# Optimization experiments

Hardware: AMD Instinct MI355X
Metric: run time of the kernel (lower is better)

## Reference

```python
import jax, jax.numpy as jnp
import numpy as np

TOP_K = 2  # cfg.MODEL.MOE.TOP_K


def setup_inputs() -> dict:
    key = jax.random.key(0)
    ks = jax.random.split(key, 5)
    bs, L, d_in, d_out, E = 32, 1024, 768, 256, 8
    return {
        "x": jax.random.normal(ks[0], (bs, L, d_in), dtype=jnp.float32),
        "gate_W": jax.random.normal(ks[1], (d_in, E), dtype=jnp.float32) * (1.0 / np.sqrt(d_in)),
        "gate_b": jax.random.normal(ks[2], (E,), dtype=jnp.float32) * 0.01,
        "expert_W": jax.random.normal(ks[3], (E, d_in, d_out), dtype=jnp.float32) * (1.0 / np.sqrt(d_in)),
        "expert_b": jax.random.normal(ks[4], (E, d_out), dtype=jnp.float32) * 0.01,
    }


def reference(x, gate_W, gate_b, expert_W, expert_b):
    # Gate: (bs, L, E) softmax over experts, then top-k routing weights.
    gate_logits = jnp.einsum("bli,ie->ble", x, gate_W) + gate_b
    gate_weights = jax.nn.softmax(gate_logits, axis=-1)
    topk_vals, topk_idx = jax.lax.top_k(gate_weights, TOP_K)  # (bs, L, K)

    # Dense all-expert projection (E is small), then gather the selected ones.
    # all_out: (bs, L, E, d_out)
    all_out = jnp.einsum("bli,eio->bleo", x, expert_W) + expert_b

    # Select top-k expert outputs per token: (bs, L, K, d_out)
    sel = jnp.take_along_axis(all_out, topk_idx[..., None], axis=2)

    # Weighted combine over the K routed experts -> (bs, L, d_out)
    output = jnp.sum(sel * topk_vals[..., None], axis=2)
    return output
```

## Files before the change

kernel.cpp:

```cpp
#include <hip/hip_runtime.h>
#include <hip/hip_bf16.h>
#include <stdint.h>

#define T_TOKENS 32768
#define D_IN     768
#define D_OUT    256
#define N_EXP    8
#define S_TOT    (T_TOKENS*2)
#define S_PAD    66560
#define NKB      24

typedef __attribute__((ext_vector_type(8))) short bf16x8;
typedef __attribute__((ext_vector_type(4))) float f32x4;

__device__ __forceinline__ unsigned short f2bf(float f) {
    unsigned u = __float_as_uint(f);
    return (unsigned short)((u + 0x7FFFu + ((u >> 16) & 1u)) >> 16);
}
__device__ __forceinline__ unsigned pack_bf2(float a, float b) {
    return (unsigned)f2bf(a) | ((unsigned)f2bf(b) << 16);
}

__device__ __forceinline__ void async16(void* lds, const void* g) {
    __builtin_amdgcn_global_load_lds(
        (const __attribute__((address_space(1))) unsigned int*)g,
        (__attribute__((address_space(3))) unsigned int*)lds, 16, 0, 0);
}

__global__ __launch_bounds__(256) void convw_kernel(
        const float* __restrict__ W, unsigned short* __restrict__ WTb,
        int* __restrict__ zero16) {
    if (blockIdx.x == 0 && threadIdx.x < 16) zero16[threadIdx.x] = 0;
    int eb_ = blockIdx.x;
    int n = threadIdx.x;
    const float* src = W + ((size_t)(eb_ / NKB) * D_IN + (eb_ % NKB) * 32) * 256 + n;
    unsigned pk[16];
    #pragma unroll
    for (int j = 0; j < 16; j++)
        pk[j] = pack_bf2(src[(2*j) * 256], src[(2*j+1) * 256]);
    unsigned* dst = (unsigned*)(WTb + ((size_t)eb_ * 256 + n) * 32);
    #pragma unroll
    for (int j = 0; j < 16; j++) dst[j] = pk[j];
}

__global__ __launch_bounds__(256) void gate_fused_kernel(
        const float* __restrict__ x, const float* __restrict__ gW,
        const float* __restrict__ gb, unsigned short* __restrict__ xbf,
        float* __restrict__ topk_w, int* __restrict__ topk_e,
        int* __restrict__ counts) {
    __shared__ float tile[32 * 133];
    __shared__ float gws[1024];
    __shared__ int h8[8];
    int tid = threadIdx.x;
    if (tid < 8) h8[tid] = 0;
    int t0 = blockIdx.x * 32;
    int kf = tid & 31, rb = tid >> 5;
    int tt = tid >> 3, qq = tid & 7;
    float acc[8] = {0,0,0,0,0,0,0,0};
    #pragma unroll 1
    for (int ch = 0; ch < 6; ++ch) {
        int kc = ch * 128;
        __syncthreads();
        *(float4*)&gws[tid * 4] = *(const float4*)(gW + kc * 8 + tid * 4);
        #pragma unroll
        for (int i = 0; i < 4; ++i) {
            int row = i * 8 + rb;
            size_t g = (size_t)(t0 + row) * D_IN + kc + kf * 4;
            float4 v = *(const float4*)(x + g);
            uint2 p; p.x = pack_bf2(v.x, v.y); p.y = pack_bf2(v.z, v.w);
            *(uint2*)(xbf + g) = p;
            float* d = &tile[row * 133 + kf * 4];
            d[0] = v.x; d[1] = v.y; d[2] = v.z; d[3] = v.w;
        }
        __syncthreads();
        #pragma unroll
        for (int kk = 0; kk < 16; ++kk) {
            float xv = tile[tt * 133 + qq + 8 * kk];
            const float* gp = &gws[(qq + 8 * kk) * 8];
            #pragma unroll
            for (int e = 0; e < 8; ++e) acc[e] += xv * gp[e];
        }
    }
    #pragma unroll
    for (int e = 0; e < 8; ++e) {
        acc[e] += __shfl_xor(acc[e], 1);
        acc[e] += __shfl_xor(acc[e], 2);
        acc[e] += __shfl_xor(acc[e], 4);
    }
    if (qq == 0) {
        int t = t0 + tt;
        float mx = -1e30f;
        #pragma unroll
        for (int e = 0; e < 8; ++e) { acc[e] += gb[e]; mx = fmaxf(mx, acc[e]); }
        float w[8], s = 0.f;
        #pragma unroll
        for (int e = 0; e < 8; ++e) { w[e] = expf(acc[e] - mx); s += w[e]; }
        float inv = 1.0f / s;
        int e0 = 0; float b0 = -1.f;
        #pragma unroll
        for (int e = 0; e < 8; ++e) if (w[e] > b0) { b0 = w[e]; e0 = e; }
        int e1 = 0; float b1 = -1.f;
        #pragma unroll
        for (int e = 0; e < 8; ++e) if (e != e0 && w[e] > b1) { b1 = w[e]; e1 = e; }
        topk_w[t*2]   = b0 * inv;
        topk_w[t*2+1] = b1 * inv;
        topk_e[t*2]   = e0;
        topk_e[t*2+1] = e1;
        atomicAdd(&h8[e0], 1); atomicAdd(&h8[e1], 1);
    }
    __syncthreads();
    if (tid < 8) atomicAdd(&counts[tid], h8[tid]);
}

__global__ void scatter_kernel(const int* __restrict__ topk_e, const float* __restrict__ topk_w,
                               const int* __restrict__ counts, int* __restrict__ cursors,
                               int* __restrict__ slot_token, float* __restrict__ slot_w,
                               int* __restrict__ inv_slot) {
    int offs[9]; offs[0] = 0;
    #pragma unroll
    for (int e = 0; e < 8; e++) offs[e+1] = offs[e] + ((counts[e] + 127) & ~127);
    if (blockIdx.x == 0) {
        #pragma unroll
        for (int e = 0; e < 8; e++) {
            int start = offs[e] + counts[e];
            for (int i = start + threadIdx.x; i < offs[e+1]; i += 256) slot_w[i] = 0.f;
        }
    }
    __shared__ int hcnt[8], hbase[8];
    if (threadIdx.x < 8) hcnt[threadIdx.x] = 0;
    __syncthreads();
    int idx[4], ee[4], lr[4];
    int base = blockIdx.x * 256 * 4 + threadIdx.x;
    #pragma unroll
    for (int j = 0; j < 4; j++) {
        idx[j] = base + j * 256;
        ee[j]  = topk_e[idx[j]];
        lr[j]  = atomicAdd(&hcnt[ee[j]], 1);
    }
    __syncthreads();
    if (threadIdx.x < 8) hbase[threadIdx.x] = atomicAdd(&cursors[threadIdx.x], hcnt[threadIdx.x]);
    __syncthreads();
    #pragma unroll
    for (int j = 0; j < 4; j++) {
        int slot = offs[ee[j]] + hbase[ee[j]] + lr[j];
        slot_token[slot] = idx[j] >> 1;
        slot_w[slot]     = topk_w[idx[j]];
        inv_slot[idx[j]] = slot;
    }
}

template<bool ROUTED>
__global__ __launch_bounds__(512, 4) void moe_gemm_kernel(
        const unsigned short* __restrict__ xbf, const unsigned short* __restrict__ WTb,
        const float* __restrict__ eb, const int* __restrict__ counts,
        const int* __restrict__ slot_token, const float* __restrict__ slot_w,
        float* __restrict__ dst) {
    __shared__ unsigned short A_lds[3][128 * 32];

    int lbid = (blockIdx.x & 7) * ((int)gridDim.x >> 3) + (blockIdx.x >> 3);

    int offs[9]; offs[0] = 0;
    #pragma unroll
    for (int e = 0; e < 8; e++) offs[e+1] = offs[e] + ((counts[e] + 127) & ~127);
    int row0 = lbid * 128;
    if (row0 >= offs[8]) return;
    int expert = 0;
    #pragma unroll
    for (int e = 0; e < 8; e++) if (row0 >= offs[e]) expert = e;

    int tid  = threadIdx.x;
    int wave = tid >> 6, lane = tid & 63;
    int lrow = lane & 15, lquad = lane >> 4;
    int wm = wave >> 2, wn = wave & 3;

    int ar = tid >> 2, ap = tid & 3;
    int alc = (ap - (ar >> 1)) & 3;
    int tok = slot_token[row0 + ar];
    tok = (tok < 0 || tok >= T_TOKENS) ? 0 : tok;
    const unsigned short* asrc = xbf + (size_t)tok * D_IN + alc * 8;

    const unsigned short* bptr = WTb + (size_t)expert * NKB * 8192
                                     + (wn * 64 + lrow) * 32 + lquad * 8;

    int a_off[4];
    #pragma unroll
    for (int m = 0; m < 4; m++) {
        int r = wm * 64 + m * 16 + lrow;
        a_off[m] = r * 32 + ((lquad + (r >> 1)) & 3) * 8;
    }

    f32x4 acc[4][4];
    #pragma unroll
    for (int m = 0; m < 4; m++)
        #pragma unroll
        for (int q = 0; q < 4; q++) acc[m][q] = (f32x4){0,0,0,0};

    bf16x8 bA[4], bB[4];
    auto bload = [&](int kb, bf16x8 (&b)[4]) {
        const unsigned short* bp = bptr + (size_t)kb * 8192;
        #pragma unroll
        for (int q = 0; q < 4; q++) b[q] = *(const bf16x8*)(bp + q * 512);
    };

    auto kstep = [&](int s, bf16x8 (&bcur)[4], bf16x8 (&bnxt)[4]) {
        if (s == NKB - 1) asm volatile("s_waitcnt vmcnt(0)" ::: "memory");
        else              asm volatile("s_waitcnt vmcnt(5)" ::: "memory");
        asm volatile("s_barrier" ::: "memory");
        if (s + 1 < NKB) bload(s + 1, bnxt);
        if (s + 2 < NKB)
            async16(&A_lds[(s + 2) % 3][tid * 8], asrc + (s + 2) * 32);
        int p = s % 3;
        bf16x8 a[4];
        #pragma unroll
        for (int m = 0; m < 4; m++) a[m] = *(const bf16x8*)&A_lds[p][a_off[m]];
        __builtin_amdgcn_s_setprio(1);
        #pragma unroll
        for (int q = 0; q < 4; q++)
            #pragma unroll
            for (int m = 0; m < 4; m++)
                acc[m][q] = __builtin_amdgcn_mfma_f32_16x16x32_bf16(a[m], bcur[q], acc[m][q], 0, 0, 0);
        __builtin_amdgcn_s_setprio(0);
    };

    async16(&A_lds[0][tid * 8], asrc);
    __builtin_amdgcn_sched_barrier(0);
    bload(0, bA);
    async16(&A_lds[1][tid * 8], asrc + 32);
    for (int s = 0; s < NKB; s += 2) {
        kstep(s, bA, bB);
        kstep(s + 1, bB, bA);
    }

    float bias_q[4];
    #pragma unroll
    for (int q = 0; q < 4; q++)
        bias_q[q] = eb[expert * D_OUT + wn * 64 + q * 16 + lrow];
    #pragma unroll
    for (int m = 0; m < 4; m++) {
        #pragma unroll
        for (int r = 0; r < 4; r++) {
            int slot = row0 + wm * 64 + m * 16 + lquad * 4 + r;
            if constexpr (ROUTED) {
                float* drow = dst + (size_t)slot * D_OUT + wn * 64;
                #pragma unroll
                for (int q = 0; q < 4; q++)
                    drow[q * 16 + lrow] = acc[m][q][r] + bias_q[q];
            } else {
                int tk = slot_token[slot];
                float wgt = slot_w[slot];
                if (wgt != 0.f) {
                    #pragma unroll
                    for (int q = 0; q < 4; q++)
                        atomicAdd(dst + (size_t)tk * D_OUT + wn * 64 + q * 16 + lrow,
                                  wgt * (acc[m][q][r] + bias_q[q]));
                }
            }
        }
    }
}

__global__ void combine_kernel(const float* __restrict__ routed, const int* __restrict__ inv_slot,
                               const float* __restrict__ topk_w, float* __restrict__ out) {
    int flat = blockIdx.x * 256 + threadIdx.x;
    int t = flat >> 6, c = (flat & 63) * 4;
    int   s0 = inv_slot[t*2], s1 = inv_slot[t*2+1];
    float w0 = topk_w[t*2],   w1 = topk_w[t*2+1];
    float4 r0 = *(const float4*)(routed + (size_t)s0 * D_OUT + c);
    float4 r1 = *(const float4*)(routed + (size_t)s1 * D_OUT + c);
    float4 o;
    o.x = w0*r0.x + w1*r1.x; o.y = w0*r0.y + w1*r1.y;
    o.z = w0*r0.z + w1*r1.z; o.w = w0*r0.w + w1*r1.w;
    *(float4*)(out + (size_t)t * D_OUT + c) = o;
}

extern "C" void kernel_launch(void* const* d_in, const int* in_sizes, int n_in,
                              void* d_out, int out_size, void* d_ws, size_t ws_size,
                              hipStream_t stream) {
    const float* x  = (const float*)d_in[0];
    const float* gW = (const float*)d_in[1];
    const float* gb = (const float*)d_in[2];
    const float* eW = (const float*)d_in[3];
    const float* eb = (const float*)d_in[4];
    float* out = (float*)d_out;
    char* ws = (char*)d_ws;

    float* topk_w      = (float*)(ws + 0);
    int*   topk_e      = (int*)  (ws + 262144);
    int*   counts      = (int*)  (ws + 524288);
    int*   cursors     = (int*)  (ws + 524320);
    int*   slot_token  = (int*)  (ws + 524416);
    float* slot_w      = (float*)(ws + 790656);
    int*   inv_slot    = (int*)  (ws + 1056896);
    unsigned short* WTb= (unsigned short*)(ws + 7610496);
    unsigned short* xbf= (unsigned short*)(ws + 10756224);
    float* routed      = (float*)(ws + 61087872);
    const size_t NEED_ROUTED = 61087872 + (size_t)S_PAD * D_OUT * 4;
    bool use_routed = (ws_size >= NEED_ROUTED);

    convw_kernel      <<<N_EXP * NKB, 256, 0, stream>>>(eW, WTb, counts);
    gate_fused_kernel <<<T_TOKENS / 32, 256, 0, stream>>>(x, gW, gb, xbf,
                                                          topk_w, topk_e, counts);
    scatter_kernel    <<<S_TOT / (256 * 4), 256, 0, stream>>>(topk_e, topk_w, counts, cursors,
                                                              slot_token, slot_w, inv_slot);
    if (use_routed) {
        moe_gemm_kernel<true><<<S_PAD / 128, 512, 0, stream>>>(xbf, WTb, eb, counts,
                                                               slot_token, slot_w, routed);
        combine_kernel<<<T_TOKENS * D_OUT / 4 / 256, 256, 0, stream>>>(routed, inv_slot,
                                                                       topk_w, out);
    } else {
        hipMemsetAsync(slot_token, 0, 532480, stream);
        hipMemsetAsync(out, 0, (size_t)out_size * sizeof(float), stream);
        moe_gemm_kernel<false><<<S_PAD / 128, 512, 0, stream>>>(xbf, WTb, eb, counts,
                                                                slot_token, slot_w, out);
    }
}
```

Measured before the change: 255.5 us.

## Repartition expert GEMM waves to 128x32 tiles and vectorize gate LDS reads

The expert GEMM changes its wave layout from a 2x4 grid of 64x64 sub-tiles to eight waves that each own all 128 rows and a 32-column slice. Each wave now loads only half as many B fragments from global memory, and the duplicate B loads across the two row-halves go away. The cost is twice as many LDS reads of the A tile per wave. The wait count drops to match the smaller number of outstanding loads, and the triple-buffer index uses rotating counters instead of modulo. The gate kernel also reads its weights from LDS as float4 vectors instead of scalar floats.

```diff
diff --git a/kernel.cpp b/kernel.cpp
--- a/kernel.cpp
+++ b/kernel.cpp
@@ -49,7 +49,7 @@
         float* __restrict__ topk_w, int* __restrict__ topk_e,
         int* __restrict__ counts) {
     __shared__ float tile[32 * 133];
-    __shared__ float gws[1024];
+    __shared__ float4 gws4[256];
     __shared__ int h8[8];
     int tid = threadIdx.x;
     if (tid < 8) h8[tid] = 0;
@@ -61,7 +61,7 @@
     for (int ch = 0; ch < 6; ++ch) {
         int kc = ch * 128;
         __syncthreads();
-        *(float4*)&gws[tid * 4] = *(const float4*)(gW + kc * 8 + tid * 4);
+        gws4[tid] = *(const float4*)(gW + kc * 8 + tid * 4);
         #pragma unroll
         for (int i = 0; i < 4; ++i) {
             int row = i * 8 + rb;
@@ -76,9 +76,12 @@
         #pragma unroll
         for (int kk = 0; kk < 16; ++kk) {
             float xv = tile[tt * 133 + qq + 8 * kk];
-            const float* gp = &gws[(qq + 8 * kk) * 8];
-            #pragma unroll
-            for (int e = 0; e < 8; ++e) acc[e] += xv * gp[e];
+            float4 g0 = gws4[(qq + 8 * kk) * 2];
+            float4 g1 = gws4[(qq + 8 * kk) * 2 + 1];
+            acc[0] += xv * g0.x; acc[1] += xv * g0.y;
+            acc[2] += xv * g0.z; acc[3] += xv * g0.w;
+            acc[4] += xv * g1.x; acc[5] += xv * g1.y;
+            acc[6] += xv * g1.z; acc[7] += xv * g1.w;
         }
     }
     #pragma unroll
@@ -171,7 +174,7 @@
     int tid  = threadIdx.x;
     int wave = tid >> 6, lane = tid & 63;
     int lrow = lane & 15, lquad = lane >> 4;
-    int wm = wave >> 2, wn = wave & 3;
+    int wn = wave;
 
     int ar = tid >> 2, ap = tid & 3;
     int alc = (ap - (ar >> 1)) & 3;
@@ -180,78 +183,84 @@
     const unsigned short* asrc = xbf + (size_t)tok * D_IN + alc * 8;
 
     const unsigned short* bptr = WTb + (size_t)expert * NKB * 8192
-                                     + (wn * 64 + lrow) * 32 + lquad * 8;
-
-    int a_off[4];
-    #pragma unroll
-    for (int m = 0; m < 4; m++) {
-        int r = wm * 64 + m * 16 + lrow;
+                                     + (wn * 32 + lrow) * 32 + lquad * 8;
+
+    int a_off[8];
+    #pragma unroll
+    for (int m = 0; m < 8; m++) {
+        int r = m * 16 + lrow;
         a_off[m] = r * 32 + ((lquad + (r >> 1)) & 3) * 8;
     }
 
-    f32x4 acc[4][4];
-    #pragma unroll
-    for (int m = 0; m < 4; m++)
-        #pragma unroll
-        for (int q = 0; q < 4; q++) acc[m][q] = (f32x4){0,0,0,0};
-
-    bf16x8 bA[4], bB[4];
-    auto bload = [&](int kb, bf16x8 (&b)[4]) {
+    f32x4 acc[8][2];
+    #pragma unroll
+    for (int m = 0; m < 8; m++)
+        #pragma unroll
+        for (int q = 0; q < 2; q++) acc[m][q] = (f32x4){0,0,0,0};
+
+    bf16x8 bA[2], bB[2];
+    auto bload = [&](int kb, bf16x8 (&b)[2]) {
         const unsigned short* bp = bptr + (size_t)kb * 8192;
         #pragma unroll
-        for (int q = 0; q < 4; q++) b[q] = *(const bf16x8*)(bp + q * 512);
+        for (int q = 0; q < 2; q++) b[q] = *(const bf16x8*)(bp + q * 512);
     };
 
-    auto kstep = [&](int s, bf16x8 (&bcur)[4], bf16x8 (&bnxt)[4]) {
+    int rd = 0, wr = 2;
+    auto kstep = [&](int s, bf16x8 (&bcur)[2], bf16x8 (&bnxt)[2]) {
         if (s == NKB - 1) asm volatile("s_waitcnt vmcnt(0)" ::: "memory");
-        else              asm volatile("s_waitcnt vmcnt(5)" ::: "memory");
+        else              asm volatile("s_waitcnt vmcnt(3)" ::: "memory");
         asm volatile("s_barrier" ::: "memory");
         if (s + 1 < NKB) bload(s + 1, bnxt);
         if (s + 2 < NKB)
-            async16(&A_lds[(s + 2) % 3][tid * 8], asrc + (s + 2) * 32);
-        int p = s % 3;
-        bf16x8 a[4];
-        #pragma unroll
-        for (int m = 0; m < 4; m++) a[m] = *(const bf16x8*)&A_lds[p][a_off[m]];
-        __builtin_amdgcn_s_setprio(1);
-        #pragma unroll
-        for (int q = 0; q < 4; q++)
+            async16(&A_lds[wr][tid * 8], asrc + (s + 2) * 32);
+        #pragma unroll
+        for (int g = 0; g < 2; ++g) {
+            bf16x8 a[4];
             #pragma unroll
-            for (int m = 0; m < 4; m++)
-                acc[m][q] = __builtin_amdgcn_mfma_f32_16x16x32_bf16(a[m], bcur[q], acc[m][q], 0, 0, 0);
-        __builtin_amdgcn_s_setprio(0);
+            for (int m = 0; m < 4; ++m) a[m] = *(const bf16x8*)&A_lds[rd][a_off[g*4+m]];
+            __builtin_amdgcn_s_setprio(1);
+            #pragma unroll
+            for (int q = 0; q < 2; ++q)
+                #pragma unroll
+                for (int m = 0; m < 4; ++m)
+                    acc[g*4+m][q] = __builtin_amdgcn_mfma_f32_16x16x32_bf16(
+                        a[m], bcur[q], acc[g*4+m][q], 0, 0, 0);
+            __builtin_amdgcn_s_setprio(0);
+        }
+        rd = rd == 2 ? 0 : rd + 1;
+        wr = wr == 2 ? 0 : wr + 1;
     };
 
     async16(&A_lds[0][tid * 8], asrc);
+    async16(&A_lds[1][tid * 8], asrc + 32);
     __builtin_amdgcn_sched_barrier(0);
     bload(0, bA);
-    async16(&A_lds[1][tid * 8], asrc + 32);
     for (int s = 0; s < NKB; s += 2) {
         kstep(s, bA, bB);
         kstep(s + 1, bB, bA);
     }
 
-    float bias_q[4];
-    #pragma unroll
-    for (int q = 0; q < 4; q++)
-        bias_q[q] = eb[expert * D_OUT + wn * 64 + q * 16 + lrow];
-    #pragma unroll
-    for (int m = 0; m < 4; m++) {
+    float bias_q[2];
+    #pragma unroll
+    for (int q = 0; q < 2; q++)
+        bias_q[q] = eb[expert * D_OUT + wn * 32 + q * 16 + lrow];
+    #pragma unroll
+    for (int m = 0; m < 8; m++) {
         #pragma unroll
         for (int r = 0; r < 4; r++) {
-            int slot = row0 + wm * 64 + m * 16 + lquad * 4 + r;
+            int slot = row0 + m * 16 + lquad * 4 + r;
             if constexpr (ROUTED) {
-                float* drow = dst + (size_t)slot * D_OUT + wn * 64;
+                float* drow = dst + (size_t)slot * D_OUT + wn * 32;
                 #pragma unroll
-                for (int q = 0; q < 4; q++)
+                for (int q = 0; q < 2; q++)
                     drow[q * 16 + lrow] = acc[m][q][r] + bias_q[q];
             } else {
                 int tk = slot_token[slot];
                 float wgt = slot_w[slot];
                 if (wgt != 0.f) {
                     #pragma unroll
-                    for (int q = 0; q < 4; q++)
-                        atomicAdd(dst + (size_t)tk * D_OUT + wn * 64 + q * 16 + lrow,
+                    for (int q = 0; q < 2; q++)
+                        atomicAdd(dst + (size_t)tk * D_OUT + wn * 32 + q * 16 + lrow,
                                   wgt * (acc[m][q][r] + bias_q[q]));
                 }
             }
```

After: 248.5 us. 1.03x faster.
